# Performance work log

Hardware: AMD Instinct MI355X
Metric: run time of the kernel (lower is better)

The kernel has to match this reference:

```python
import jax, jax.numpy as jnp
import numpy as np

N_SRC = 50000
N_DST = 50000
E = 800000
D = 128
K = 8  # args.k: number of randomly sampled neighbors


def setup_inputs() -> dict:
    key = jax.random.key(0)
    k1, k2, k3, k4, k5, k6 = jax.random.split(key, 6)
    h_src = jax.random.normal(k1, (N_SRC, D), dtype=jnp.float32)
    h_dst = jax.random.normal(k2, (N_DST, D), dtype=jnp.float32)
    unif = jax.random.uniform(k3, (N_DST, K), dtype=jnp.float32)
    src_idx = jax.random.randint(k4, (E,), 0, N_SRC, dtype=jnp.int32)
    dst_idx = jnp.sort(jax.random.randint(k5, (E,), 0, N_DST, dtype=jnp.int32))
    category = jax.random.randint(k6, (N_SRC,), 0, 50, dtype=jnp.int32)
    return {"h_src": h_src, "h_dst": h_dst, "unif": unif,
            "src_idx": src_idx, "dst_idx": dst_idx, "category": category}


def _forward(h_src, h_dst, unif, src_idx, dst_idx, category):
    n_src = h_src.shape[0]
    n_dst = h_dst.shape[0]
    e = src_idx.shape[0]
    ones = jnp.ones((e,), dtype=h_src.dtype)

    # src-side symmetric norm: feat_src * out_deg^-0.5
    out_deg = jax.ops.segment_sum(ones, src_idx, num_segments=n_src)
    out_norm = jnp.clip(out_deg, 1.0, None) ** -0.5
    feat_src = h_src * out_norm[:, None]

    # mailbox gather: message per edge m_e = feat_src[src_e]  -> [E, D]
    msg = feat_src[src_idx]

    # in-degrees and full segment-sum reduction
    in_deg = jax.ops.segment_sum(ones, dst_idx, num_segments=n_dst)
    full_sum = jax.ops.segment_sum(msg, dst_idx, num_segments=n_dst)  # [N_dst, D]

    # random neighbor subsampling with replacement (dst_idx is sorted):
    # node n owns edges [ptr[n], ptr[n]+deg[n]); pick K offsets via floor(u*deg)
    deg_i = in_deg.astype(jnp.int32)
    ptr = jnp.searchsorted(dst_idx, jnp.arange(n_dst, dtype=jnp.int32), side="left").astype(jnp.int32)
    off = jnp.floor(unif * in_deg[:, None]).astype(jnp.int32)
    off = jnp.minimum(off, jnp.maximum(deg_i[:, None] - 1, 0))  # guard u==1 / deg==0
    eid = jnp.clip(ptr[:, None] + off, 0, e - 1)                # [N_dst, K]
    samp_sum = msg[eid].sum(axis=1)                              # [N_dst, D]

    # bucket escape hatch: any incoming category == -1 -> sum everything
    neg_in = jax.ops.segment_sum((category[src_idx] == -1).astype(jnp.int32),
                                 dst_idx, num_segments=n_dst)
    use_full = (deg_i <= K) | (neg_in > 0)
    rst = jnp.where(use_full[:, None], full_sum, samp_sum)

    # dst-side norm: rst * in_deg^-0.5
    in_norm = jnp.clip(in_deg, 1.0, None) ** -0.5
    return rst * in_norm[:, None]


def reference(h_src, h_dst, unif, src_idx, dst_idx, category):
    return _forward(h_src, h_dst, unif, src_idx, dst_idx, category)
```

## Files before the change

kernel.cpp:

```cpp
#include <hip/hip_runtime.h>

#define N_SRC 50000
#define N_DST 50000
#define E_CNT 800000
#define D 128
#define K 8
#define NSHADOW 8

#define CNT_THREADS (E_CNT / 4)
#define CNT_BLOCKS ((CNT_THREADS + 255) / 256)
#define PTR_BLOCKS ((N_DST + 1 + 255) / 256)


__device__ __forceinline__ int xcc_id() {
    int x;
    asm("s_getreg_b32 %0, hwreg(HW_REG_XCC_ID)" : "=s"(x));
    return x & (NSHADOW - 1);
}

__device__ __forceinline__ void atomic_add_xcd(int* p, int v) {
    asm volatile("global_atomic_add %0, %1, off" :: "v"(p), "v"(v) : "memory");
}

__global__ void count_ptr_kernel(const int* __restrict__ src_idx,
                                 const int* __restrict__ dst_idx,
                                 const int* __restrict__ category,
                                 int* __restrict__ shadow,
                                 int* __restrict__ neg_in,
                                 int* __restrict__ ptr) {
    if (blockIdx.x < CNT_BLOCKS) {
        int t = blockIdx.x * 256 + threadIdx.x;
        if (t >= CNT_THREADS) return;
        int* sh = shadow + (size_t)xcc_id() * N_SRC;
        int4 s = ((const int4*)src_idx)[t];
        atomic_add_xcd(&sh[s.x], 1);
        atomic_add_xcd(&sh[s.y], 1);
        atomic_add_xcd(&sh[s.z], 1);
        atomic_add_xcd(&sh[s.w], 1);
        if (category[s.x] == -1) atomicAdd(&neg_in[dst_idx[4 * t + 0]], 1);
        if (category[s.y] == -1) atomicAdd(&neg_in[dst_idx[4 * t + 1]], 1);
        if (category[s.z] == -1) atomicAdd(&neg_in[dst_idx[4 * t + 2]], 1);
        if (category[s.w] == -1) atomicAdd(&neg_in[dst_idx[4 * t + 3]], 1);
    } else {
        int n = (blockIdx.x - CNT_BLOCKS) * 256 + threadIdx.x;
        if (n > N_DST) return;
        int lo = 0, hi = E_CNT;
        while (lo < hi) {
            int mid = (lo + hi) >> 1;
            if (dst_idx[mid] < n) lo = mid + 1; else hi = mid;
        }
        ptr[n] = lo;
    }
}

__global__ void reduce_norm_kernel(const int* __restrict__ shadow,
                                   float* __restrict__ out_norm) {
    int n = blockIdx.x * blockDim.x + threadIdx.x;
    if (n >= N_SRC) return;
    int d = 0;
    #pragma unroll
    for (int x = 0; x < NSHADOW; ++x) d += shadow[(size_t)x * N_SRC + n];
    out_norm[n] = rsqrtf((float)max(d, 1));
}

__global__ void gather_kernel(const float* __restrict__ h_src,
                              const float* __restrict__ unif,
                              const int* __restrict__ src_idx,
                              const float* __restrict__ out_norm,
                              const int* __restrict__ neg_in,
                              const int* __restrict__ ptr,
                              float* __restrict__ out) {
    int gid = blockIdx.x * blockDim.x + threadIdx.x;
    int n = gid >> 6;
    int lane = threadIdx.x & 63;
    if (n >= N_DST) return;

    int p = ptr[n];
    int deg = ptr[n + 1] - p;
    bool use_full = (deg <= K) || (neg_in[n] > 0);

    const float2* h2 = (const float2*)h_src;
    float2 acc = make_float2(0.f, 0.f);

    if (use_full) {
        for (int i = 0; i < deg; ++i) {
            int s = src_idx[p + i];
            float norm = out_norm[s];
            float2 v = h2[(size_t)s * 64 + lane];
            acc.x += v.x * norm;
            acc.y += v.y * norm;
        }
    } else {
        int s_k = 0;
        if (lane < K) {
            float u = unif[n * K + lane];
            int off = (int)floorf(u * (float)deg);
            if (off > deg - 1) off = deg - 1;
            if (off < 0) off = 0;
            int eid = p + off;
            if (eid < 0) eid = 0;
            if (eid > E_CNT - 1) eid = E_CNT - 1;
            s_k = src_idx[eid];
        }
        #pragma unroll
        for (int k = 0; k < K; ++k) {
            int s = __shfl(s_k, k, 64);
            float norm = out_norm[s];
            float2 v = h2[(size_t)s * 64 + lane];
            acc.x += v.x * norm;
            acc.y += v.y * norm;
        }
    }

    float in_norm = rsqrtf((float)max(deg, 1));
    float2 r;
    r.x = acc.x * in_norm;
    r.y = acc.y * in_norm;
    ((float2*)out)[(size_t)n * 64 + lane] = r;
}

extern "C" void kernel_launch(void* const* d_in, const int* in_sizes, int n_in,
                              void* d_out, int out_size, void* d_ws, size_t ws_size,
                              hipStream_t stream) {
    const float* h_src   = (const float*)d_in[0];
    const float* unif    = (const float*)d_in[2];
    const int* src_idx   = (const int*)d_in[3];
    const int* dst_idx   = (const int*)d_in[4];
    const int* category  = (const int*)d_in[5];
    float* out = (float*)d_out;

    int* shadow    = (int*)d_ws;
    int* neg_in    = shadow + (size_t)NSHADOW * N_SRC;
    int* ptr       = neg_in + N_DST;
    float* out_norm = (float*)(ptr + N_DST + 1);

    hipMemsetAsync(shadow, 0, ((size_t)NSHADOW * N_SRC + N_DST) * sizeof(int), stream);

    count_ptr_kernel<<<CNT_BLOCKS + PTR_BLOCKS, 256, 0, stream>>>(
        src_idx, dst_idx, category, shadow, neg_in, ptr);

    reduce_norm_kernel<<<(N_SRC + 255) / 256, 256, 0, stream>>>(shadow, out_norm);

    {
        int threads = 256;
        long long total = (long long)N_DST * 64;
        int blocks = (int)((total + threads - 1) / threads);
        gather_kernel<<<blocks, threads, 0, stream>>>(h_src, unif, src_idx,
                                                      out_norm, neg_in,
                                                      ptr, out);
    }
}
```

Measured before the change: 162.5 us.

## Replace global atomic out-degree histogram with per-block LDS histograms in two passes

Out-degree counting moves from global atomics into per-XCC shadow arrays to 64 blocks, each building a shared-memory histogram. Counts are packed as two 16-bit values per word, and the source range is covered in two halves so the histogram fits in LDS. Each block writes a private slab that the reduce kernel sums over 64 slabs. This removes global atomic traffic and the large memset. In exchange there is much less parallelism in the histogram phase, each block reads src_idx twice, the reduce step has many more slab reads, and a 16-bit count would overflow if any block saw more than 65535 hits for one source.

After: 145.6 us. -10.4%, faster.

```diff
diff --git a/kernel.cpp b/kernel.cpp
--- a/kernel.cpp
+++ b/kernel.cpp
@@ -5,44 +5,57 @@
 #define E_CNT 800000
 #define D 128
 #define K 8
-#define NSHADOW 8
 
-#define CNT_THREADS (E_CNT / 4)
-#define CNT_BLOCKS ((CNT_THREADS + 255) / 256)
-#define PTR_BLOCKS ((N_DST + 1 + 255) / 256)
+#define HIST_BLOCKS 64
+#define HIST_THREADS 512
+#define PTR_BLOCKS ((N_DST + 1 + HIST_THREADS - 1) / HIST_THREADS)
+#define HALF 25000
+#define HWORDS (HALF / 2)
+#define NCHUNK (E_CNT / 4)
 
 
-__device__ __forceinline__ int xcc_id() {
-    int x;
-    asm("s_getreg_b32 %0, hwreg(HW_REG_XCC_ID)" : "=s"(x));
-    return x & (NSHADOW - 1);
-}
+__global__ __launch_bounds__(HIST_THREADS)
+void count_ptr_kernel(const int* __restrict__ src_idx,
+                      const int* __restrict__ dst_idx,
+                      const int* __restrict__ category,
+                      int* __restrict__ slab,
+                      int* __restrict__ neg_in,
+                      int* __restrict__ ptr) {
+    if (blockIdx.x < HIST_BLOCKS) {
+        __shared__ int hist[HWORDS];
+        const int4* s4 = (const int4*)src_idx;
+        int* myslab = slab + (size_t)blockIdx.x * N_SRC;
 
-__device__ __forceinline__ void atomic_add_xcd(int* p, int v) {
-    asm volatile("global_atomic_add %0, %1, off" :: "v"(p), "v"(v) : "memory");
-}
+        for (int pass = 0; pass < 2; ++pass) {
+            int base = pass * HALF;
+            for (int j = threadIdx.x; j < HWORDS; j += HIST_THREADS) hist[j] = 0;
+            __syncthreads();
 
-__global__ void count_ptr_kernel(const int* __restrict__ src_idx,
-                                 const int* __restrict__ dst_idx,
-                                 const int* __restrict__ category,
-                                 int* __restrict__ shadow,
-                                 int* __restrict__ neg_in,
-                                 int* __restrict__ ptr) {
-    if (blockIdx.x < CNT_BLOCKS) {
-        int t = blockIdx.x * 256 + threadIdx.x;
-        if (t >= CNT_THREADS) return;
-        int* sh = shadow + (size_t)xcc_id() * N_SRC;
-        int4 s = ((const int4*)src_idx)[t];
-        atomic_add_xcd(&sh[s.x], 1);
-        atomic_add_xcd(&sh[s.y], 1);
-        atomic_add_xcd(&sh[s.z], 1);
-        atomic_add_xcd(&sh[s.w], 1);
-        if (category[s.x] == -1) atomicAdd(&neg_in[dst_idx[4 * t + 0]], 1);
-        if (category[s.y] == -1) atomicAdd(&neg_in[dst_idx[4 * t + 1]], 1);
-        if (category[s.z] == -1) atomicAdd(&neg_in[dst_idx[4 * t + 2]], 1);
-        if (category[s.w] == -1) atomicAdd(&neg_in[dst_idx[4 * t + 3]], 1);
+            for (int c = blockIdx.x * HIST_THREADS + threadIdx.x; c < NCHUNK;
+                 c += HIST_BLOCKS * HIST_THREADS) {
+                int4 s = s4[c];
+                int r;
+                r = s.x - base; if ((unsigned)r < HALF) atomicAdd(&hist[r >> 1], 1 << ((r & 1) * 16));
+                r = s.y - base; if ((unsigned)r < HALF) atomicAdd(&hist[r >> 1], 1 << ((r & 1) * 16));
+                r = s.z - base; if ((unsigned)r < HALF) atomicAdd(&hist[r >> 1], 1 << ((r & 1) * 16));
+                r = s.w - base; if ((unsigned)r < HALF) atomicAdd(&hist[r >> 1], 1 << ((r & 1) * 16));
+                if (pass == 0) {
+                    if (category[s.x] == -1) atomicAdd(&neg_in[dst_idx[4 * c + 0]], 1);
+                    if (category[s.y] == -1) atomicAdd(&neg_in[dst_idx[4 * c + 1]], 1);
+                    if (category[s.z] == -1) atomicAdd(&neg_in[dst_idx[4 * c + 2]], 1);
+                    if (category[s.w] == -1) atomicAdd(&neg_in[dst_idx[4 * c + 3]], 1);
+                }
+            }
+            __syncthreads();
+
+            for (int j = threadIdx.x; j < HWORDS; j += HIST_THREADS) {
+                unsigned w = (unsigned)hist[j];
+                ((int2*)(myslab + base))[j] = make_int2((int)(w & 0xffffu), (int)(w >> 16));
+            }
+            __syncthreads();
+        }
     } else {
-        int n = (blockIdx.x - CNT_BLOCKS) * 256 + threadIdx.x;
+        int n = (blockIdx.x - HIST_BLOCKS) * HIST_THREADS + threadIdx.x;
         if (n > N_DST) return;
         int lo = 0, hi = E_CNT;
         while (lo < hi) {
@@ -53,13 +66,13 @@
     }
 }
 
-__global__ void reduce_norm_kernel(const int* __restrict__ shadow,
+__global__ void reduce_norm_kernel(const int* __restrict__ slab,
                                    float* __restrict__ out_norm) {
     int n = blockIdx.x * blockDim.x + threadIdx.x;
     if (n >= N_SRC) return;
     int d = 0;
     #pragma unroll
-    for (int x = 0; x < NSHADOW; ++x) d += shadow[(size_t)x * N_SRC + n];
+    for (int b = 0; b < HIST_BLOCKS; ++b) d += slab[(size_t)b * N_SRC + n];
     out_norm[n] = rsqrtf((float)max(d, 1));
 }
 
@@ -129,17 +142,17 @@
     const int* category  = (const int*)d_in[5];
     float* out = (float*)d_out;
 
-    int* shadow    = (int*)d_ws;
-    int* neg_in    = shadow + (size_t)NSHADOW * N_SRC;
+    int* slab      = (int*)d_ws;
+    int* neg_in    = slab + (size_t)HIST_BLOCKS * N_SRC;
     int* ptr       = neg_in + N_DST;
     float* out_norm = (float*)(ptr + N_DST + 1);
 
-    hipMemsetAsync(shadow, 0, ((size_t)NSHADOW * N_SRC + N_DST) * sizeof(int), stream);
+    hipMemsetAsync(neg_in, 0, (size_t)N_DST * sizeof(int), stream);
 
-    count_ptr_kernel<<<CNT_BLOCKS + PTR_BLOCKS, 256, 0, stream>>>(
-        src_idx, dst_idx, category, shadow, neg_in, ptr);
+    count_ptr_kernel<<<HIST_BLOCKS + PTR_BLOCKS, HIST_THREADS, 0, stream>>>(
+        src_idx, dst_idx, category, slab, neg_in, ptr);
 
-    reduce_norm_kernel<<<(N_SRC + 255) / 256, 256, 0, stream>>>(shadow, out_norm);
+    reduce_norm_kernel<<<(N_SRC + 255) / 256, 256, 0, stream>>>(slab, out_norm);
 
     {
         int threads = 256;
```
